# Optimization experiments

Measured on AMD Instinct MI355X. Metric: run time of the kernel, lower is better.

Reference implementation:

```python
import jax, jax.numpy as jnp
import numpy as np

N, F, C, H = 6144, 128, 64, 4
NEG = -1.0e10


def setup_inputs() -> dict:
    key = jax.random.key(0)
    ks = jax.random.split(key, 8)
    X = jax.random.normal(ks[0], (N, F), dtype=jnp.float32)
    A = (jax.random.uniform(ks[1], (N, N)) < 0.01).astype(jnp.float32)  # sparse-ish 0/1 adjacency
    A = A.at[jnp.arange(N), jnp.arange(N)].set(1.0)  # self loops so every row has a neighbor
    s = 1.0 / np.sqrt(F)
    W1 = jax.random.normal(ks[2], (H, F, C), dtype=jnp.float32) * s
    W2 = jax.random.normal(ks[3], (H, F, C), dtype=jnp.float32) * s
    a_self = jax.random.normal(ks[4], (H, C), dtype=jnp.float32) * (1.0 / np.sqrt(C))
    a_neigh = jax.random.normal(ks[5], (H, C), dtype=jnp.float32) * (1.0 / np.sqrt(C))
    bias = jnp.zeros((H, C), dtype=jnp.float32)
    return {"X": X, "A": A, "W1": W1, "W2": W2, "a_self": a_self, "a_neigh": a_neigh, "bias": bias}


def reference(X, A, W1, W2, a_self, a_neigh, bias):
    # Per-head projections: [H, N, C]
    feats = jnp.einsum('nf,hfc->hnc', X, W1)
    feats2 = jnp.einsum('nf,hfc->hnc', X, W2)
    # Attention logits: self term + transposed neighbor term -> [H, N, N]
    att_s = jnp.einsum('hnc,hc->hn', feats, a_self)
    att_n = jnp.einsum('hnc,hc->hn', feats, a_neigh)
    dense = att_s[:, :, None] + att_n[:, None, :]
    dense = jnp.where(dense > 0, dense, 0.2 * dense)  # LeakyReLU(0.2)
    dense = dense + NEG * (1.0 - A)[None, :, :]       # additive adjacency mask
    attn = jax.nn.softmax(dense, axis=-1)
    # Dropout layers are identity at inference.
    node = jnp.einsum('hnm,hmc->hnc', attn, feats) + feats2 + bias[:, None, :]
    out = jnp.mean(node, axis=0)  # attn_heads_reduction='average'
    return jax.nn.relu(out)
```

## Files before the change

kernel.cpp:

```cpp
#include <hip/hip_runtime.h>
#include <hip/hip_bf16.h>


#define N_NODES 6144
#define F_DIM   128
#define C_DIM   64
#define H_HEADS 4
#define HC      (H_HEADS * C_DIM)
#define MAXKW   128

typedef unsigned short u16;
typedef float v4f __attribute__((ext_vector_type(4)));

__global__ __launch_bounds__(256) void proj_kernel(
    const float* __restrict__ X,
    const float* __restrict__ W1, const float* __restrict__ W2,
    const float* __restrict__ a_self, const float* __restrict__ a_neigh,
    u16* __restrict__ featsB, float* __restrict__ feats2T,
    float* __restrict__ attsT, float* __restrict__ attnT)
{
    const int rt    = blockIdx.x;
    const int z     = blockIdx.y;
    const int h     = z >> 1;
    const int which = z & 1;

    const float* W = (which ? W2 : W1) + h * F_DIM * C_DIM;

    __shared__ float  Xs[64][132];
    __shared__ float4 Ws4[128][17];

    const int tid = threadIdx.x;

    {
        const float4* Xg = (const float4*)(X + (size_t)rt * 64 * F_DIM);
        for (int u = tid; u < 64 * 32; u += 256) {
            const int r = u >> 5, q = u & 31;
            *(float4*)&Xs[r][4 * q] = Xg[u];
        }
        const float4* Wg = (const float4*)W;
        for (int u = tid; u < 128 * 16; u += 256) {
            Ws4[u >> 4][u & 15] = Wg[u];
        }
    }
    __syncthreads();

    const int tx = tid & 15;
    const int ty = tid >> 4;

    float acc[4][4] = {};
    for (int k = 0; k < 128; k += 4) {
        const float4 b0 = Ws4[k + 0][tx];
        const float4 b1 = Ws4[k + 1][tx];
        const float4 b2 = Ws4[k + 2][tx];
        const float4 b3 = Ws4[k + 3][tx];
        #pragma unroll
        for (int i = 0; i < 4; ++i) {
            const float4 x = *(const float4*)&Xs[4 * ty + i][k];
            acc[i][0] += x.x * b0.x + x.y * b1.x + x.z * b2.x + x.w * b3.x;
            acc[i][1] += x.x * b0.y + x.y * b1.y + x.z * b2.y + x.w * b3.y;
            acc[i][2] += x.x * b0.z + x.y * b1.z + x.z * b2.z + x.w * b3.z;
            acc[i][3] += x.x * b0.w + x.y * b1.w + x.z * b2.w + x.w * b3.w;
        }
    }

    __syncthreads();
    float* Ct = &Xs[0][0];

    #pragma unroll
    for (int i = 0; i < 4; ++i) {
        const int r    = 4 * ty + i;
        const int node = rt * 64 + r;
        if (which == 0) {
            u16 p0 = __bfloat16_as_ushort(__float2bfloat16(acc[i][0]));
            u16 p1 = __bfloat16_as_ushort(__float2bfloat16(acc[i][1]));
            u16 p2 = __bfloat16_as_ushort(__float2bfloat16(acc[i][2]));
            u16 p3 = __bfloat16_as_ushort(__float2bfloat16(acc[i][3]));
            ushort4 pk; pk.x = p0; pk.y = p1; pk.z = p2; pk.w = p3;
            *(ushort4*)&featsB[(size_t)node * HC + h * C_DIM + 4 * tx] = pk;
            Ct[r * 65 + 4 * tx + 0] = acc[i][0];
            Ct[r * 65 + 4 * tx + 1] = acc[i][1];
            Ct[r * 65 + 4 * tx + 2] = acc[i][2];
            Ct[r * 65 + 4 * tx + 3] = acc[i][3];
        } else {
            *(float4*)&feats2T[(size_t)node * HC + h * C_DIM + 4 * tx] =
                make_float4(acc[i][0], acc[i][1], acc[i][2], acc[i][3]);
        }
    }

    if (which == 0) {
        __syncthreads();
        if (tid < 64) {
            const float* as_ = a_self  + h * C_DIM;
            const float* an_ = a_neigh + h * C_DIM;
            float s = 0.f, n = 0.f;
            #pragma unroll 8
            for (int c = 0; c < C_DIM; ++c) {
                const float v = Ct[tid * 65 + c];
                s += v * as_[c];
                n += v * an_[c];
            }
            const int node = rt * 64 + tid;
            attsT[node * H_HEADS + h] = s;
            attnT[node * H_HEADS + h] = n;
        }
    }
}

__global__ __launch_bounds__(256) void agg_kernel(
    const float* __restrict__ A,
    const u16* __restrict__ featsB, const float* __restrict__ feats2T,
    const float* __restrict__ attsT, const float* __restrict__ attnT,
    const float* __restrict__ bias,
    float* __restrict__ out)
{
    const int w    = threadIdx.x >> 6;
    const int lane = threadIdx.x & 63;
    const int i    = blockIdx.x * 4 + w;

    __shared__ int    idxs[4][MAXKW];
    __shared__ float4 ewsT4[4][MAXKW];
    int*    idx_w = idxs[w];
    float4* ews_w = ewsT4[w];

    const v4f* Arow = (const v4f*)(A + (size_t)i * N_NODES);
    const unsigned long long ltmask = (1ull << lane) - 1ull;
    int base = 0;
    #pragma unroll
    for (int ch = 0; ch < 4; ++ch) {
        v4f v[6];
        #pragma unroll
        for (int g = 0; g < 6; ++g)
            v[g] = __builtin_nontemporal_load(Arow + lane + 64 * (ch * 6 + g));
        #pragma unroll
        for (int g = 0; g < 6; ++g) {
            const int col = 4 * (lane + 64 * (ch * 6 + g));
            #pragma unroll
            for (int m = 0; m < 4; ++m) {
                const float x = (m == 0) ? v[g].x : (m == 1) ? v[g].y
                              : (m == 2) ? v[g].z : v[g].w;
                const bool p = (x > 0.5f);
                const unsigned long long mask = __ballot(p);
                if (p) {
                    const int pos = base + (int)__popcll(mask & ltmask);
                    if (pos < MAXKW) idx_w[pos] = col + m;
                }
                base += (int)__popcll(mask);
            }
        }
    }
    const int K = min(base, MAXKW);

    const float4 si4 = ((const float4*)attsT)[i];
    float zx = 0.f, zy = 0.f, zz = 0.f, zw = 0.f;
    #pragma unroll
    for (int r = 0; r < 2; ++r) {
        const int k = lane + 64 * r;
        if (k < K) {
            const float4 an = ((const float4*)attnT)[idx_w[k]];
            float l;
            float4 e4;
            l = si4.x + an.x; e4.x = __expf((l > 0.f) ? l : 0.2f * l);
            l = si4.y + an.y; e4.y = __expf((l > 0.f) ? l : 0.2f * l);
            l = si4.z + an.z; e4.z = __expf((l > 0.f) ? l : 0.2f * l);
            l = si4.w + an.w; e4.w = __expf((l > 0.f) ? l : 0.2f * l);
            ews_w[k] = e4;
            zx += e4.x; zy += e4.y; zz += e4.z; zw += e4.w;
        }
    }
    #pragma unroll
    for (int off = 32; off > 0; off >>= 1) {
        zx += __shfl_xor(zx, off);
        zy += __shfl_xor(zy, off);
        zz += __shfl_xor(zz, off);
        zw += __shfl_xor(zw, off);
    }
    const int hsel = lane >> 4;
    const float zinv = 1.0f / ((hsel == 0) ? zx : (hsel == 1) ? zy
                             : (hsel == 2) ? zz : zw);

    const uint2* fb = (const uint2*)featsB;
    float a0 = 0.f, a1 = 0.f, a2 = 0.f, a3 = 0.f;

    #define UPFMA(q, wgt)                                                   \
        {                                                                   \
            const float f0 = __uint_as_float((q).x << 16);                  \
            const float f1 = __uint_as_float((q).x & 0xffff0000u);          \
            const float f2 = __uint_as_float((q).y << 16);                  \
            const float f3 = __uint_as_float((q).y & 0xffff0000u);          \
            a0 += (wgt) * f0; a1 += (wgt) * f1;                             \
            a2 += (wgt) * f2; a3 += (wgt) * f3;                             \
        }

    int k = 0;
    for (; k + 8 <= K; k += 8) {
        const int4 j0 = *(const int4*)&idx_w[k];
        const int4 j1 = *(const int4*)&idx_w[k + 4];
        const float w0 = ((const float*)&ews_w[k + 0])[hsel];
        const float w1 = ((const float*)&ews_w[k + 1])[hsel];
        const float w2 = ((const float*)&ews_w[k + 2])[hsel];
        const float w3 = ((const float*)&ews_w[k + 3])[hsel];
        const float w4 = ((const float*)&ews_w[k + 4])[hsel];
        const float w5 = ((const float*)&ews_w[k + 5])[hsel];
        const float w6 = ((const float*)&ews_w[k + 6])[hsel];
        const float w7 = ((const float*)&ews_w[k + 7])[hsel];
        const uint2 q0 = fb[(size_t)j0.x * 64 + lane];
        const uint2 q1 = fb[(size_t)j0.y * 64 + lane];
        const uint2 q2 = fb[(size_t)j0.z * 64 + lane];
        const uint2 q3 = fb[(size_t)j0.w * 64 + lane];
        const uint2 q4 = fb[(size_t)j1.x * 64 + lane];
        const uint2 q5 = fb[(size_t)j1.y * 64 + lane];
        const uint2 q6 = fb[(size_t)j1.z * 64 + lane];
        const uint2 q7 = fb[(size_t)j1.w * 64 + lane];
        UPFMA(q0, w0) UPFMA(q1, w1) UPFMA(q2, w2) UPFMA(q3, w3)
        UPFMA(q4, w4) UPFMA(q5, w5) UPFMA(q6, w6) UPFMA(q7, w7)
    }
    for (; k < K; ++k) {
        const int   j  = idx_w[k];
        const float wg = ((const float*)&ews_w[k])[hsel];
        const uint2 q  = fb[(size_t)j * 64 + lane];
        UPFMA(q, wg)
    }
    #undef UPFMA

    const float4 f2 = *(const float4*)&feats2T[(size_t)i * HC + 4 * lane];
    const float4 b4 = *(const float4*)&bias[4 * lane];
    float s0 = a0 * zinv + f2.x + b4.x;
    float s1 = a1 * zinv + f2.y + b4.y;
    float s2 = a2 * zinv + f2.z + b4.z;
    float s3 = a3 * zinv + f2.w + b4.w;
    s0 += __shfl_xor(s0, 16); s0 += __shfl_xor(s0, 32);
    s1 += __shfl_xor(s1, 16); s1 += __shfl_xor(s1, 32);
    s2 += __shfl_xor(s2, 16); s2 += __shfl_xor(s2, 32);
    s3 += __shfl_xor(s3, 16); s3 += __shfl_xor(s3, 32);
    if (lane < 16) {
        float4 o;
        o.x = fmaxf(0.25f * s0, 0.f);
        o.y = fmaxf(0.25f * s1, 0.f);
        o.z = fmaxf(0.25f * s2, 0.f);
        o.w = fmaxf(0.25f * s3, 0.f);
        *(float4*)&out[(size_t)i * C_DIM + 4 * lane] = o;
    }
}

extern "C" void kernel_launch(void* const* d_in, const int* in_sizes, int n_in,
                              void* d_out, int out_size, void* d_ws, size_t ws_size,
                              hipStream_t stream) {
    const float* X       = (const float*)d_in[0];
    const float* A       = (const float*)d_in[1];
    const float* W1      = (const float*)d_in[2];
    const float* W2      = (const float*)d_in[3];
    const float* a_self  = (const float*)d_in[4];
    const float* a_neigh = (const float*)d_in[5];
    const float* bias    = (const float*)d_in[6];
    float* out = (float*)d_out;

    float* ws      = (float*)d_ws;
    float* feats2T = ws;
    float* attsT   = feats2T + (size_t)N_NODES * HC;
    float* attnT   = attsT   + (size_t)N_NODES * H_HEADS;
    u16*   featsB  = (u16*)(attnT + (size_t)N_NODES * H_HEADS);

    dim3 grid1(N_NODES / 64, H_HEADS * 2);
    proj_kernel<<<grid1, 256, 0, stream>>>(X, W1, W2, a_self, a_neigh,
                                           featsB, feats2T, attsT, attnT);

    agg_kernel<<<N_NODES / 4, 256, 0, stream>>>(A, featsB, feats2T, attsT, attnT, bias, out);
}
```

Measured before the change: 245.5 us.

## Merge W1/W2 projections per block, shuffle-reduce logits, double-buffer adjacency loads

The projection kernel now handles one head per block and computes both W1 and W2 products, so the X tile is loaded once and reused. The attention logits are reduced with warp shuffles in registers instead of a shared-memory pass by 64 threads. In the aggregation kernel, loads of the adjacency row are double-buffered so the next chunk is fetched while the current one is compacted, and the prefix count uses mbcnt intrinsics. The trade-off is half as many projection blocks and more registers held live for the prefetch.

New measurement: 246.5 us. About the same (+0.4%).

```diff
diff --git a/kernel.cpp b/kernel.cpp
--- a/kernel.cpp
+++ b/kernel.cpp
@@ -19,17 +19,15 @@
     u16* __restrict__ featsB, float* __restrict__ feats2T,
     float* __restrict__ attsT, float* __restrict__ attnT)
 {
-    const int rt    = blockIdx.x;
-    const int z     = blockIdx.y;
-    const int h     = z >> 1;
-    const int which = z & 1;
-
-    const float* W = (which ? W2 : W1) + h * F_DIM * C_DIM;
+    const int rt = blockIdx.x;
+    const int h  = blockIdx.y;
 
     __shared__ float  Xs[64][132];
-    __shared__ float4 Ws4[128][17];
+    __shared__ float4 Ws4[128][16];
 
     const int tid = threadIdx.x;
+    const int tx  = tid & 15;
+    const int ty  = tid >> 4;
 
     {
         const float4* Xg = (const float4*)(X + (size_t)rt * 64 * F_DIM);
@@ -37,72 +35,74 @@
             const int r = u >> 5, q = u & 31;
             *(float4*)&Xs[r][4 * q] = Xg[u];
         }
-        const float4* Wg = (const float4*)W;
-        for (int u = tid; u < 128 * 16; u += 256) {
+        const float4* Wg = (const float4*)(W1 + (size_t)h * F_DIM * C_DIM);
+        for (int u = tid; u < 128 * 16; u += 256)
             Ws4[u >> 4][u & 15] = Wg[u];
-        }
     }
     __syncthreads();
 
-    const int tx = tid & 15;
-    const int ty = tid >> 4;
+#define MM_LOOP(ACC)                                                        \
+    for (int k = 0; k < 128; k += 4) {                                      \
+        const float4 b0 = Ws4[k + 0][tx];                                   \
+        const float4 b1 = Ws4[k + 1][tx];                                   \
+        const float4 b2 = Ws4[k + 2][tx];                                   \
+        const float4 b3 = Ws4[k + 3][tx];                                   \
+        _Pragma("unroll")                                                   \
+        for (int i = 0; i < 4; ++i) {                                       \
+            const float4 x = *(const float4*)&Xs[4 * ty + i][k];            \
+            ACC[i][0] += x.x * b0.x + x.y * b1.x + x.z * b2.x + x.w * b3.x; \
+            ACC[i][1] += x.x * b0.y + x.y * b1.y + x.z * b2.y + x.w * b3.y; \
+            ACC[i][2] += x.x * b0.z + x.y * b1.z + x.z * b2.z + x.w * b3.z; \
+            ACC[i][3] += x.x * b0.w + x.y * b1.w + x.z * b2.w + x.w * b3.w; \
+        }                                                                   \
+    }
 
     float acc[4][4] = {};
-    for (int k = 0; k < 128; k += 4) {
-        const float4 b0 = Ws4[k + 0][tx];
-        const float4 b1 = Ws4[k + 1][tx];
-        const float4 b2 = Ws4[k + 2][tx];
-        const float4 b3 = Ws4[k + 3][tx];
-        #pragma unroll
-        for (int i = 0; i < 4; ++i) {
-            const float4 x = *(const float4*)&Xs[4 * ty + i][k];
-            acc[i][0] += x.x * b0.x + x.y * b1.x + x.z * b2.x + x.w * b3.x;
-            acc[i][1] += x.x * b0.y + x.y * b1.y + x.z * b2.y + x.w * b3.y;
-            acc[i][2] += x.x * b0.z + x.y * b1.z + x.z * b2.z + x.w * b3.z;
-            acc[i][3] += x.x * b0.w + x.y * b1.w + x.z * b2.w + x.w * b3.w;
-        }
-    }
-
-    __syncthreads();
-    float* Ct = &Xs[0][0];
-
+    MM_LOOP(acc)
+
+    const float4 asv = *(const float4*)&a_self[h * C_DIM + 4 * tx];
+    const float4 anv = *(const float4*)&a_neigh[h * C_DIM + 4 * tx];
     #pragma unroll
     for (int i = 0; i < 4; ++i) {
-        const int r    = 4 * ty + i;
-        const int node = rt * 64 + r;
-        if (which == 0) {
-            u16 p0 = __bfloat16_as_ushort(__float2bfloat16(acc[i][0]));
-            u16 p1 = __bfloat16_as_ushort(__float2bfloat16(acc[i][1]));
-            u16 p2 = __bfloat16_as_ushort(__float2bfloat16(acc[i][2]));
-            u16 p3 = __bfloat16_as_ushort(__float2bfloat16(acc[i][3]));
-            ushort4 pk; pk.x = p0; pk.y = p1; pk.z = p2; pk.w = p3;
-            *(ushort4*)&featsB[(size_t)node * HC + h * C_DIM + 4 * tx] = pk;
-            Ct[r * 65 + 4 * tx + 0] = acc[i][0];
-            Ct[r * 65 + 4 * tx + 1] = acc[i][1];
-            Ct[r * 65 + 4 * tx + 2] = acc[i][2];
-            Ct[r * 65 + 4 * tx + 3] = acc[i][3];
-        } else {
-            *(float4*)&feats2T[(size_t)node * HC + h * C_DIM + 4 * tx] =
-                make_float4(acc[i][0], acc[i][1], acc[i][2], acc[i][3]);
-        }
-    }
-
-    if (which == 0) {
-        __syncthreads();
-        if (tid < 64) {
-            const float* as_ = a_self  + h * C_DIM;
-            const float* an_ = a_neigh + h * C_DIM;
-            float s = 0.f, n = 0.f;
-            #pragma unroll 8
-            for (int c = 0; c < C_DIM; ++c) {
-                const float v = Ct[tid * 65 + c];
-                s += v * as_[c];
-                n += v * an_[c];
-            }
-            const int node = rt * 64 + tid;
+        const int node = rt * 64 + 4 * ty + i;
+        ushort4 pk;
+        pk.x = __bfloat16_as_ushort(__float2bfloat16(acc[i][0]));
+        pk.y = __bfloat16_as_ushort(__float2bfloat16(acc[i][1]));
+        pk.z = __bfloat16_as_ushort(__float2bfloat16(acc[i][2]));
+        pk.w = __bfloat16_as_ushort(__float2bfloat16(acc[i][3]));
+        *(ushort4*)&featsB[(size_t)node * HC + h * C_DIM + 4 * tx] = pk;
+
+        float s = acc[i][0] * asv.x + acc[i][1] * asv.y
+                + acc[i][2] * asv.z + acc[i][3] * asv.w;
+        float n = acc[i][0] * anv.x + acc[i][1] * anv.y
+                + acc[i][2] * anv.z + acc[i][3] * anv.w;
+        s += __shfl_xor(s, 1); s += __shfl_xor(s, 2);
+        s += __shfl_xor(s, 4); s += __shfl_xor(s, 8);
+        n += __shfl_xor(n, 1); n += __shfl_xor(n, 2);
+        n += __shfl_xor(n, 4); n += __shfl_xor(n, 8);
+        if (tx == 0) {
             attsT[node * H_HEADS + h] = s;
             attnT[node * H_HEADS + h] = n;
         }
+    }
+
+    __syncthreads();
+    {
+        const float4* Wg = (const float4*)(W2 + (size_t)h * F_DIM * C_DIM);
+        for (int u = tid; u < 128 * 16; u += 256)
+            Ws4[u >> 4][u & 15] = Wg[u];
+    }
+    __syncthreads();
+
+    float acc2[4][4] = {};
+    MM_LOOP(acc2)
+#undef MM_LOOP
+
+    #pragma unroll
+    for (int i = 0; i < 4; ++i) {
+        const int node = rt * 64 + 4 * ty + i;
+        *(float4*)&feats2T[(size_t)node * HC + h * C_DIM + 4 * tx] =
+            make_float4(acc2[i][0], acc2[i][1], acc2[i][2], acc2[i][3]);
     }
 }
 
@@ -123,25 +123,36 @@
     float4* ews_w = ewsT4[w];
 
     const v4f* Arow = (const v4f*)(A + (size_t)i * N_NODES);
-    const unsigned long long ltmask = (1ull << lane) - 1ull;
     int base = 0;
+
+    v4f va[6], vb[6];
+    #pragma unroll
+    for (int g = 0; g < 6; ++g)
+        va[g] = __builtin_nontemporal_load(Arow + lane + 64 * g);
+
     #pragma unroll
     for (int ch = 0; ch < 4; ++ch) {
-        v4f v[6];
-        #pragma unroll
-        for (int g = 0; g < 6; ++g)
-            v[g] = __builtin_nontemporal_load(Arow + lane + 64 * (ch * 6 + g));
+        v4f* cur = (ch & 1) ? vb : va;
+        v4f* nxt = (ch & 1) ? va : vb;
+        if (ch < 3) {
+            #pragma unroll
+            for (int g = 0; g < 6; ++g)
+                nxt[g] = __builtin_nontemporal_load(Arow + lane + 64 * ((ch + 1) * 6 + g));
+        }
         #pragma unroll
         for (int g = 0; g < 6; ++g) {
             const int col = 4 * (lane + 64 * (ch * 6 + g));
             #pragma unroll
             for (int m = 0; m < 4; ++m) {
-                const float x = (m == 0) ? v[g].x : (m == 1) ? v[g].y
-                              : (m == 2) ? v[g].z : v[g].w;
+                const float x = (m == 0) ? cur[g].x : (m == 1) ? cur[g].y
+                              : (m == 2) ? cur[g].z : cur[g].w;
                 const bool p = (x > 0.5f);
                 const unsigned long long mask = __ballot(p);
                 if (p) {
-                    const int pos = base + (int)__popcll(mask & ltmask);
+                    const int below = __builtin_amdgcn_mbcnt_hi(
+                        (unsigned int)(mask >> 32),
+                        __builtin_amdgcn_mbcnt_lo((unsigned int)mask, 0u));
+                    const int pos = base + below;
                     if (pos < MAXKW) idx_w[pos] = col + m;
                 }
                 base += (int)__popcll(mask);
@@ -260,7 +271,7 @@
     float* attnT   = attsT   + (size_t)N_NODES * H_HEADS;
     u16*   featsB  = (u16*)(attnT + (size_t)N_NODES * H_HEADS);
 
-    dim3 grid1(N_NODES / 64, H_HEADS * 2);
+    dim3 grid1(N_NODES / 64, H_HEADS);
     proj_kernel<<<grid1, 256, 0, stream>>>(X, W1, W2, a_self, a_neigh,
                                            featsB, feats2T, attsT, attnT);
 
```
